# Optimization experiments

Measured on AMD Instinct MI355X. Metric: run time of the kernel, lower is better.

## Reference

```python
import jax, jax.numpy as jnp
import numpy as np

NUM_ATOMS = 100
D = 32        # initial_atom_dim
H = 16        # hidden_dim (multiplicity per irrep)
NB = 16       # edge_dim / number of bessel basis functions
CUT = 6.0     # radius_cutoff
DEG = 4.0     # degree_norm
OUT = 1       # output_dim
INV4PI = 1.0 / np.sqrt(4.0 * np.pi)  # 'integral' SH normalization


def _bessel(d, nb, cut):
    # e3nn soft_one_hot_linspace(basis='bessel', cutoff=True) * sqrt(nb)
    x = d[:, None]
    n = jnp.arange(1, nb + 1, dtype=d.dtype)
    safe = jnp.maximum(x, 1e-9)
    out = np.sqrt(2.0 / cut) * jnp.sin(n * jnp.pi * x / cut) / safe
    return out * (x < cut) * np.sqrt(float(nb))


def _fc(x, w1, w2):
    # e3nn FullyConnectedNet: fan-in normalized linear layers, silu, no bias
    h = jax.nn.silu(x @ w1 / np.sqrt(x.shape[-1]))
    return h @ w2 / np.sqrt(w1.shape[-1])


def _forward(atomic_numbers, edge_index, coords, atom_emb,
             fc0_w1, fc0_w2, fc1_w1, fc1_w2, w_readout):
    src, dst = edge_index[0], edge_index[1]
    N = coords.shape[0]
    E = src.shape[0]

    vec = coords[src] - coords[dst]                      # [E,3]
    dist = jnp.linalg.norm(vec, axis=-1)                 # [E]
    unit = vec / jnp.maximum(dist, 1e-9)[:, None]

    # spherical harmonics, l=0 and l=1, 'integral' normalization
    y0 = jnp.full((E,), INV4PI, dtype=coords.dtype)      # [E]
    y1 = (np.sqrt(3.0) * INV4PI) * unit                  # [E,3]
    basis = _bessel(dist, NB, CUT)                       # [E,NB]

    x = atom_emb[atomic_numbers]                         # [N,D] (row 0 is padding)

    # ---- layer 0: scalars (D x0e) x (1x0e+1x1o) -> H x0e + H x1o ----
    w = _fc(basis, fc0_w1, fc0_w2)                       # [E, 2*D*H] per-edge TP weights
    wa = w[:, : D * H].reshape(E, D, H)
    wb = w[:, D * H:].reshape(E, D, H)
    xs = x[src]
    n0 = 1.0 / np.sqrt(D)                                # path fan-in norm
    m0 = jnp.einsum('ed,edh->eh', xs, wa) * y0[:, None] * n0          # [E,H]
    m1 = jnp.einsum('ed,edh->eh', xs, wb)[:, :, None] * y1[:, None, :] * n0  # [E,H,3]
    z0 = jax.ops.segment_sum(m0, dst, num_segments=N) / DEG           # [N,H]
    z1 = jax.ops.segment_sum(m1, dst, num_segments=N) / DEG           # [N,H,3]

    # ---- layer 1: (H x0e + H x1o) x (1x0e+1x1o) -> same irreps, skip-connected ----
    w = _fc(basis, fc1_w1, fc1_w2)                       # [E, 4*H*H]
    w1_ = w[:, 0 * H * H:1 * H * H].reshape(E, H, H)     # 0e x 0e -> 0e
    w2_ = w[:, 1 * H * H:2 * H * H].reshape(E, H, H)     # 0e x 1o -> 1o
    w3_ = w[:, 2 * H * H:3 * H * H].reshape(E, H, H)     # 1o x 0e -> 1o
    w4_ = w[:, 3 * H * H:4 * H * H].reshape(E, H, H)     # 1o x 1o -> 0e (CG = dot/sqrt(3))
    s, v = z0[src], z1[src]
    n1 = 1.0 / np.sqrt(2 * H)                            # two paths per output irrep
    dot = jnp.einsum('ehm,em->eh', v, y1) / np.sqrt(3.0)
    o0 = (jnp.einsum('eh,ehk->ek', s, w1_) * y0[:, None]
          + jnp.einsum('eh,ehk->ek', dot, w4_)) * n1
    o1 = (jnp.einsum('eh,ehk->ek', s, w2_)[:, :, None] * y1[:, None, :]
          + jnp.einsum('ehm,ehk->ekm', v, w3_) * y0[:, None, None]) * n1
    z0 = jax.ops.segment_sum(o0, dst, num_segments=N) / DEG + z0      # skip
    z1 = jax.ops.segment_sum(o1, dst, num_segments=N) / DEG + z1

    # ---- scalar readout (o3.Linear onto 0e) + graph sum-pool ----
    node_scalar = z0 @ w_readout / np.sqrt(H)            # [N,OUT]
    return jnp.sum(node_scalar, axis=0)                  # [OUT]


def setup_inputs() -> dict:
    key = jax.random.key(0)
    ks = jax.random.split(key, 9)
    N, E = 10000, 160000
    atomic_numbers = jax.random.randint(ks[0], (N,), 0, NUM_ATOMS)
    coords = jax.random.normal(ks[1], (N, 3), dtype=jnp.float32)
    edge_index = jax.random.randint(ks[2], (2, E), 0, N)
    atom_emb = jax.random.normal(ks[3], (NUM_ATOMS, D), dtype=jnp.float32).at[0].set(0.0)
    fc0_w1 = jax.random.normal(ks[4], (NB, H), dtype=jnp.float32)
    fc0_w2 = jax.random.normal(ks[5], (H, 2 * D * H), dtype=jnp.float32)
    fc1_w1 = jax.random.normal(ks[6], (NB, H), dtype=jnp.float32)
    fc1_w2 = jax.random.normal(ks[7], (H, 4 * H * H), dtype=jnp.float32)
    w_readout = jax.random.normal(ks[8], (H, OUT), dtype=jnp.float32)
    return {"atomic_numbers": atomic_numbers, "coords": coords, "edge_index": edge_index,
            "atom_emb": atom_emb, "fc0_w1": fc0_w1, "fc0_w2": fc0_w2,
            "fc1_w1": fc1_w1, "fc1_w2": fc1_w2, "w_readout": w_readout}


def reference(atomic_numbers, coords, edge_index, atom_emb,
              fc0_w1, fc0_w2, fc1_w1, fc1_w2, w_readout):
    return _forward(atomic_numbers, edge_index, coords, atom_emb,
                    fc0_w1, fc0_w2, fc1_w1, fc1_w2, w_readout)
```

## Files before the change

### kernel.cpp

```cpp
#include <hip/hip_runtime.h>
#include <math.h>


namespace {
constexpr int   NATOMS   = 100;
constexpr int   CAP      = 64;
constexpr float PI_F     = 3.14159265358979323846f;
constexpr float INV4PI_F = 0.28209479177387814f;
constexpr float SQRT3_F  = 1.7320508075688772f;
constexpr float CUT_F    = 6.0f;
constexpr float BASIS_C  = 2.3094010767585034f;
constexpr float N0_F     = 0.17677669529663687f;
constexpr float K0_F = INV4PI_F * N0_F * 0.0625f;
constexpr float K1_F = SQRT3_F * INV4PI_F * N0_F * 0.0625f;
}

__device__ __forceinline__ float silu_fast(float x) {
  return x / (1.0f + __expf(-x));
}

__device__ __forceinline__ float block_reduce_sum(float v) {
  #pragma unroll
  for (int o = 32; o > 0; o >>= 1) v += __shfl_down(v, o, 64);
  __shared__ float ls[8];
  int lane = threadIdx.x & 63;
  int w    = threadIdx.x >> 6;
  if (lane == 0) ls[w] = v;
  __syncthreads();
  float s = 0.f;
  if (threadIdx.x == 0) {
    int nw = (blockDim.x + 63) >> 6;
    for (int i = 0; i < nw; ++i) s += ls[i];
  }
  return s;
}

__global__ void setup_kernel(const float* __restrict__ atom_emb,
                             const float* __restrict__ fc0_w2,
                             const float* __restrict__ fc1_w2,
                             const float* __restrict__ w_readout,
                             const int* __restrict__ ei,
                             const float* __restrict__ coords,
                             const int* __restrict__ an,
                             float* __restrict__ T0, float* __restrict__ T1,
                             float* __restrict__ G1T, float* __restrict__ G4T,
                             int* __restrict__ cursor,
                             float4* __restrict__ evec,
                             float4* __restrict__ ebuf,
                             int* __restrict__ ea,
                             int E) {
  int b = blockIdx.x;
  int tt = threadIdx.x;
  if (b < NATOMS) {
    int j = tt >> 4;
    int h = tt & 15;
    float s0 = 0.f, s1 = 0.f;
    #pragma unroll
    for (int d = 0; d < 32; ++d) {
      float x = atom_emb[b * 32 + d];
      s0 = fmaf(x, fc0_w2[j * 1024 + d * 16 + h], s0);
      s1 = fmaf(x, fc0_w2[j * 1024 + 512 + d * 16 + h], s1);
    }
    T0[b * 256 + tt] = s0;
    T1[b * 256 + tt] = s1;
  } else if (b == NATOMS) {
    int j = tt >> 4;
    int h = tt & 15;
    float g1 = 0.f, g4 = 0.f;
    #pragma unroll
    for (int k = 0; k < 16; ++k) {
      float r = w_readout[k];
      g1 = fmaf(fc1_w2[j * 1024 + h * 16 + k], r, g1);
      g4 = fmaf(fc1_w2[j * 1024 + 768 + h * 16 + k], r, g4);
    }
    G1T[h * 16 + j] = g1;
    G4T[h * 16 + j] = g4;
  } else {
    int e = (b - NATOMS - 1) * blockDim.x + tt;
    if (e < E) {
      int s = ei[e];
      int d = ei[E + e];
      float vx = coords[3 * s + 0] - coords[3 * d + 0];
      float vy = coords[3 * s + 1] - coords[3 * d + 1];
      float vz = coords[3 * s + 2] - coords[3 * d + 2];
      float dist = sqrtf(vx * vx + vy * vy + vz * vz);
      float inv  = 1.0f / fmaxf(dist, 1e-9f);
      float4 rec = make_float4(vx * inv, vy * inv, vz * inv, dist);
      evec[e] = rec;
      int pos = atomicAdd(&cursor[d], 1);
      if (pos < CAP) {
        ebuf[d * CAP + pos] = rec;
        ea[d * CAP + pos]   = an[s];
      }
    }
  }
}

__global__ void __launch_bounds__(256, 4)
gather_kernel(const float4* __restrict__ ebuf,
              const int* __restrict__ ea,
              const int* __restrict__ cursor,
              const float* __restrict__ fc0_w1,
              const float* __restrict__ T0,
              const float* __restrict__ T1,
              const float* __restrict__ G1T,
              const float* __restrict__ G4T,
              const float* __restrict__ w_readout,
              float* __restrict__ zbuf,
              float* __restrict__ out,
              int N) {
  __shared__ float ggs[512];
  ggs[threadIdx.x]       = G1T[threadIdx.x];
  ggs[256 + threadIdx.x] = G4T[threadIdx.x];
  __syncthreads();

  int wave = threadIdx.x >> 6;
  int lane = threadIdx.x & 63;
  int g    = lane >> 4;
  int t    = lane & 15;
  int base = lane & 48;
  int node = blockIdx.x * 4 + wave;
  bool valid = node < N;

  float w0c[16];
  #pragma unroll
  for (int k = 0; k < 16; ++k) w0c[k] = fc0_w1[k * 16 + t];
  float rr = w_readout[t];

  int cnt = valid ? min(cursor[node], CAP) : 0;
  int nb  = (valid ? node : 0) * CAP;

  const float angc = PI_F / CUT_F;
  float acc0 = 0.f, accx = 0.f, accy = 0.f, accz = 0.f;

  for (int i = g; i < cnt; i += 4) {
    float4 ev = ebuf[nb + i];
    int    a  = ea[nb + i];
    float dist = ev.w;
    float bc = (dist < CUT_F) ? (BASIS_C / fmaxf(dist, 1e-9f)) : 0.0f;

    float ang = angc * dist;
    float sc = __sinf(ang);
    float tw = 2.0f * __cosf(ang);
    float sp = 0.f, acc = 0.f;
    #pragma unroll
    for (int k = 0; k < 16; ++k) {
      acc = fmaf(sc, w0c[k], acc);
      float sn = fmaf(tw, sc, -sp);
      sp = sc; sc = sn;
    }
    float h0t = silu_fast(acc * bc * 0.25f);

    const float* t0 = T0 + a * 256 + t;
    const float* t1 = T1 + a * 256 + t;
    float u0 = 0.f, u1 = 0.f;
    #pragma unroll
    for (int j = 0; j < 16; ++j) {
      float hj = __shfl(h0t, base + j, 64);
      u0 = fmaf(hj, t0[j * 16], u0);
      u1 = fmaf(hj, t1[j * 16], u1);
    }
    acc0 += u0;
    accx = fmaf(u1, ev.x, accx);
    accy = fmaf(u1, ev.y, accy);
    accz = fmaf(u1, ev.z, accz);
  }

  acc0 += __shfl_xor(acc0, 16, 64); acc0 += __shfl_xor(acc0, 32, 64);
  accx += __shfl_xor(accx, 16, 64); accx += __shfl_xor(accx, 32, 64);
  accy += __shfl_xor(accy, 16, 64); accy += __shfl_xor(accy, 32, 64);
  accz += __shfl_xor(accz, 16, 64); accz += __shfl_xor(accz, 32, 64);

  float srcv = (g == 0) ? acc0 * K0_F
                        : ((g == 1) ? accx : (g == 2) ? accy : accz) * K1_F;
  int tofs = (g == 0) ? 0 : 256;
  float o = 0.f;
  #pragma unroll
  for (int h = 0; h < 16; ++h) {
    float vh = __shfl(srcv, base + h, 64);
    o = fmaf(ggs[tofs + h * 16 + t], vh, o);
  }
  if (valid) zbuf[(size_t)node * 64 + t * 4 + g] = o;

  float p = (valid && g == 0) ? acc0 * K0_F * rr : 0.f;
  float tot = block_reduce_sum(p);
  if (threadIdx.x == 0) atomicAdd(out, tot * 0.25f);
}

__global__ void __launch_bounds__(256, 4)
phase2_kernel(const int* __restrict__ ei,
              const float4* __restrict__ evec,
              const float* __restrict__ fc1_w1,
              const float* __restrict__ zbuf,
              float* __restrict__ out,
              int E) {
  int t = threadIdx.x & 15;
  float w1c[16];
  #pragma unroll
  for (int k = 0; k < 16; ++k) w1c[k] = fc1_w1[k * 16 + t];

  int gid = (blockIdx.x * blockDim.x + threadIdx.x) >> 4;
  int ngroups = (gridDim.x * blockDim.x) >> 4;
  const float angc = PI_F / CUT_F;

  float c = 0.f;
  for (int e = gid; e < E; e += ngroups) {
    int s = ei[e];
    float4 ev = evec[e];
    float dist = ev.w;
    float bc = (dist < CUT_F) ? (BASIS_C / fmaxf(dist, 1e-9f)) : 0.0f;

    float ang = angc * dist;
    float sc = __sinf(ang);
    float tw = 2.0f * __cosf(ang);
    float sp = 0.f, acc = 0.f;
    #pragma unroll
    for (int k = 0; k < 16; ++k) {
      acc = fmaf(sc, w1c[k], acc);
      float sn = fmaf(tw, sc, -sp);
      sp = sc; sc = sn;
    }
    float h1t = silu_fast(acc * bc * 0.25f);

    float4 z = ((const float4*)(zbuf + (size_t)s * 64))[t];
    c = fmaf(h1t, fmaf(z.y, ev.x, fmaf(z.z, ev.y, fmaf(z.w, ev.z, z.x))), c);
  }
  c *= INV4PI_F * N0_F * (1.0f / 64.0f);
  float tot = block_reduce_sum(c);
  if (threadIdx.x == 0) atomicAdd(out, tot);
}

extern "C" void kernel_launch(void* const* d_in, const int* in_sizes, int n_in,
                              void* d_out, int out_size, void* d_ws, size_t ws_size,
                              hipStream_t stream) {
  const int*   an        = (const int*)d_in[0];
  const float* coords    = (const float*)d_in[1];
  const int*   ei        = (const int*)d_in[2];
  const float* atom_emb  = (const float*)d_in[3];
  const float* fc0_w1    = (const float*)d_in[4];
  const float* fc0_w2    = (const float*)d_in[5];
  const float* fc1_w1    = (const float*)d_in[6];
  const float* fc1_w2    = (const float*)d_in[7];
  const float* w_readout = (const float*)d_in[8];

  int N = in_sizes[0];
  int E = in_sizes[2] / 2;

  float*  ws   = (float*)d_ws;
  float*  zbuf = ws;
  float4* evec = (float4*)(zbuf + (size_t)N * 64);
  float4* ebuf = evec + E;
  float*  T0   = (float*)(ebuf + (size_t)N * CAP);
  float*  T1   = T0 + NATOMS * 256;
  float*  G1T  = T1 + NATOMS * 256;
  float*  G4T  = G1T + 256;
  int*    cursor = (int*)(G4T + 256);
  int*    ea     = cursor + N;
  float*  out = (float*)d_out;

  hipMemsetAsync(cursor, 0, (size_t)N * sizeof(int), stream);
  hipMemsetAsync(out, 0, sizeof(float), stream);

  int blk = 256;
  int ebkts = (E + blk - 1) / blk;
  setup_kernel<<<NATOMS + 1 + ebkts, blk, 0, stream>>>(
      atom_emb, fc0_w2, fc1_w2, w_readout, ei, coords, an,
      T0, T1, G1T, G4T, cursor, evec, ebuf, ea, E);

  gather_kernel<<<(N + 3) / 4, blk, 0, stream>>>(
      ebuf, ea, cursor, fc0_w1, T0, T1, G1T, G4T, w_readout, zbuf, out, N);

  phase2_kernel<<<2048, blk, 0, stream>>>(ei, evec, fc1_w1, zbuf, out, E);
}
```

Baseline: 161.5 us.

## Split layer-0 message computation into edge-parallel kernel with per-node index gather

Per-edge layer-0 messages (Bessel basis, radial MLP, atom-type contraction, SH scaling) are computed in a new edge-parallel kernel and written to a per-edge message buffer. The node kernel then gathers these messages by edge index instead of recomputing them per node. The two per-type tables are interleaved into one float2-readable table. This aims to remove per-node load imbalance and underused lanes, at the cost of an extra launch and a large intermediate buffer round trip through memory.

```diff
diff --git a/kernel.cpp b/kernel.cpp
--- a/kernel.cpp
+++ b/kernel.cpp
@@ -42,12 +42,12 @@
                              const int* __restrict__ ei,
                              const float* __restrict__ coords,
                              const int* __restrict__ an,
-                             float* __restrict__ T0, float* __restrict__ T1,
+                             float* __restrict__ TI,
                              float* __restrict__ G1T, float* __restrict__ G4T,
                              int* __restrict__ cursor,
                              float4* __restrict__ evec,
-                             float4* __restrict__ ebuf,
                              int* __restrict__ ea,
+                             int* __restrict__ elist,
                              int E) {
   int b = blockIdx.x;
   int tt = threadIdx.x;
@@ -61,8 +61,8 @@
       s0 = fmaf(x, fc0_w2[j * 1024 + d * 16 + h], s0);
       s1 = fmaf(x, fc0_w2[j * 1024 + 512 + d * 16 + h], s1);
     }
-    T0[b * 256 + tt] = s0;
-    T1[b * 256 + tt] = s1;
+    TI[b * 512 + j * 32 + 2 * h]     = s0;
+    TI[b * 512 + j * 32 + 2 * h + 1] = s1;
   } else if (b == NATOMS) {
     int j = tt >> 4;
     int h = tt & 15;
@@ -85,30 +85,81 @@
       float vz = coords[3 * s + 2] - coords[3 * d + 2];
       float dist = sqrtf(vx * vx + vy * vy + vz * vz);
       float inv  = 1.0f / fmaxf(dist, 1e-9f);
-      float4 rec = make_float4(vx * inv, vy * inv, vz * inv, dist);
-      evec[e] = rec;
+      evec[e] = make_float4(vx * inv, vy * inv, vz * inv, dist);
+      ea[e] = an[s];
       int pos = atomicAdd(&cursor[d], 1);
-      if (pos < CAP) {
-        ebuf[d * CAP + pos] = rec;
-        ea[d * CAP + pos]   = an[s];
+      if (pos < CAP) elist[d * CAP + pos] = e;
+    }
+  }
+}
+
+__global__ void __launch_bounds__(256)
+m_kernel(const float4* __restrict__ evec,
+         const int* __restrict__ ea,
+         const float* __restrict__ TI,
+         const float* __restrict__ fc0_w1,
+         float4* __restrict__ mbuf,
+         int E) {
+  __shared__ float w1s[256];
+  w1s[threadIdx.x] = fc0_w1[threadIdx.x];
+  __syncthreads();
+  int lane = threadIdx.x & 63;
+  int g    = threadIdx.x >> 4;
+  int t    = threadIdx.x & 15;
+  int base = lane & 48;
+
+  float w0c[16];
+  #pragma unroll
+  for (int k = 0; k < 16; ++k) w0c[k] = w1s[k * 16 + t];
+
+  const float angc = PI_F / CUT_F;
+  int e = blockIdx.x * 32 + g;
+  #pragma unroll
+  for (int rep = 0; rep < 2; ++rep, e += 16) {
+    if (e < E) {
+      float4 ev = evec[e];
+      int    a  = ea[e];
+      float dist = ev.w;
+      float bc = (dist < CUT_F) ? (BASIS_C / fmaxf(dist, 1e-9f)) : 0.0f;
+
+      float ang = angc * dist;
+      float sc = __sinf(ang);
+      float tw = 2.0f * __cosf(ang);
+      float sp = 0.f, acc = 0.f;
+      #pragma unroll
+      for (int k = 0; k < 16; ++k) {
+        acc = fmaf(sc, w0c[k], acc);
+        float sn = fmaf(tw, sc, -sp);
+        sp = sc; sc = sn;
       }
+      float h0t = silu_fast(acc * bc * 0.25f);
+
+      const float2* tp = (const float2*)(TI + a * 512) + t;
+      float u0 = 0.f, u1 = 0.f;
+      #pragma unroll
+      for (int j = 0; j < 16; ++j) {
+        float hj = __shfl(h0t, base + j, 64);
+        float2 T = tp[j * 16];
+        u0 = fmaf(hj, T.x, u0);
+        u1 = fmaf(hj, T.y, u1);
+      }
+      float m1 = K1_F * u1;
+      mbuf[(size_t)e * 16 + t] =
+          make_float4(K0_F * u0, m1 * ev.x, m1 * ev.y, m1 * ev.z);
     }
   }
 }
 
 __global__ void __launch_bounds__(256, 4)
-gather_kernel(const float4* __restrict__ ebuf,
-              const int* __restrict__ ea,
-              const int* __restrict__ cursor,
-              const float* __restrict__ fc0_w1,
-              const float* __restrict__ T0,
-              const float* __restrict__ T1,
-              const float* __restrict__ G1T,
-              const float* __restrict__ G4T,
-              const float* __restrict__ w_readout,
-              float* __restrict__ zbuf,
-              float* __restrict__ out,
-              int N) {
+node_kernel(const int* __restrict__ elist,
+            const int* __restrict__ cursor,
+            const float4* __restrict__ mbuf,
+            const float* __restrict__ G1T,
+            const float* __restrict__ G4T,
+            const float* __restrict__ w_readout,
+            float* __restrict__ zbuf,
+            float* __restrict__ out,
+            int N) {
   __shared__ float ggs[512];
   ggs[threadIdx.x]       = G1T[threadIdx.x];
   ggs[256 + threadIdx.x] = G4T[threadIdx.x];
@@ -122,57 +173,23 @@
   int node = blockIdx.x * 4 + wave;
   bool valid = node < N;
 
-  float w0c[16];
-  #pragma unroll
-  for (int k = 0; k < 16; ++k) w0c[k] = fc0_w1[k * 16 + t];
   float rr = w_readout[t];
-
   int cnt = valid ? min(cursor[node], CAP) : 0;
-  int nb  = (valid ? node : 0) * CAP;
-
-  const float angc = PI_F / CUT_F;
-  float acc0 = 0.f, accx = 0.f, accy = 0.f, accz = 0.f;
-
+  const int* eb = elist + (size_t)(valid ? node : 0) * CAP;
+
+  float a0 = 0.f, ax = 0.f, ay = 0.f, az = 0.f;
   for (int i = g; i < cnt; i += 4) {
-    float4 ev = ebuf[nb + i];
-    int    a  = ea[nb + i];
-    float dist = ev.w;
-    float bc = (dist < CUT_F) ? (BASIS_C / fmaxf(dist, 1e-9f)) : 0.0f;
-
-    float ang = angc * dist;
-    float sc = __sinf(ang);
-    float tw = 2.0f * __cosf(ang);
-    float sp = 0.f, acc = 0.f;
-    #pragma unroll
-    for (int k = 0; k < 16; ++k) {
-      acc = fmaf(sc, w0c[k], acc);
-      float sn = fmaf(tw, sc, -sp);
-      sp = sc; sc = sn;
-    }
-    float h0t = silu_fast(acc * bc * 0.25f);
-
-    const float* t0 = T0 + a * 256 + t;
-    const float* t1 = T1 + a * 256 + t;
-    float u0 = 0.f, u1 = 0.f;
-    #pragma unroll
-    for (int j = 0; j < 16; ++j) {
-      float hj = __shfl(h0t, base + j, 64);
-      u0 = fmaf(hj, t0[j * 16], u0);
-      u1 = fmaf(hj, t1[j * 16], u1);
-    }
-    acc0 += u0;
-    accx = fmaf(u1, ev.x, accx);
-    accy = fmaf(u1, ev.y, accy);
-    accz = fmaf(u1, ev.z, accz);
-  }
-
-  acc0 += __shfl_xor(acc0, 16, 64); acc0 += __shfl_xor(acc0, 32, 64);
-  accx += __shfl_xor(accx, 16, 64); accx += __shfl_xor(accx, 32, 64);
-  accy += __shfl_xor(accy, 16, 64); accy += __shfl_xor(accy, 32, 64);
-  accz += __shfl_xor(accz, 16, 64); accz += __shfl_xor(accz, 32, 64);
-
-  float srcv = (g == 0) ? acc0 * K0_F
-                        : ((g == 1) ? accx : (g == 2) ? accy : accz) * K1_F;
+    int eidx = eb[i];
+    float4 f = mbuf[(size_t)eidx * 16 + t];
+    a0 += f.x; ax += f.y; ay += f.z; az += f.w;
+  }
+
+  a0 += __shfl_xor(a0, 16, 64); a0 += __shfl_xor(a0, 32, 64);
+  ax += __shfl_xor(ax, 16, 64); ax += __shfl_xor(ax, 32, 64);
+  ay += __shfl_xor(ay, 16, 64); ay += __shfl_xor(ay, 32, 64);
+  az += __shfl_xor(az, 16, 64); az += __shfl_xor(az, 32, 64);
+
+  float srcv = (g == 0) ? a0 : ((g == 1) ? ax : (g == 2) ? ay : az);
   int tofs = (g == 0) ? 0 : 256;
   float o = 0.f;
   #pragma unroll
@@ -182,7 +199,7 @@
   }
   if (valid) zbuf[(size_t)node * 64 + t * 4 + g] = o;
 
-  float p = (valid && g == 0) ? acc0 * K0_F * rr : 0.f;
+  float p = (valid && g == 0) ? a0 * rr : 0.f;
   float tot = block_reduce_sum(p);
   if (threadIdx.x == 0) atomicAdd(out, tot * 0.25f);
 }
@@ -246,16 +263,15 @@
   int N = in_sizes[0];
   int E = in_sizes[2] / 2;
 
-  float*  ws   = (float*)d_ws;
-  float*  zbuf = ws;
-  float4* evec = (float4*)(zbuf + (size_t)N * 64);
-  float4* ebuf = evec + E;
-  float*  T0   = (float*)(ebuf + (size_t)N * CAP);
-  float*  T1   = T0 + NATOMS * 256;
-  float*  G1T  = T1 + NATOMS * 256;
+  float4* evec = (float4*)d_ws;
+  float4* mbuf = evec + E;
+  float*  zbuf = (float*)(mbuf + (size_t)E * 16);
+  float*  TI   = zbuf + (size_t)N * 64;
+  float*  G1T  = TI + NATOMS * 512;
   float*  G4T  = G1T + 256;
   int*    cursor = (int*)(G4T + 256);
   int*    ea     = cursor + N;
+  int*    elist  = ea + E;
   float*  out = (float*)d_out;
 
   hipMemsetAsync(cursor, 0, (size_t)N * sizeof(int), stream);
@@ -265,10 +281,12 @@
   int ebkts = (E + blk - 1) / blk;
   setup_kernel<<<NATOMS + 1 + ebkts, blk, 0, stream>>>(
       atom_emb, fc0_w2, fc1_w2, w_readout, ei, coords, an,
-      T0, T1, G1T, G4T, cursor, evec, ebuf, ea, E);
-
-  gather_kernel<<<(N + 3) / 4, blk, 0, stream>>>(
-      ebuf, ea, cursor, fc0_w1, T0, T1, G1T, G4T, w_readout, zbuf, out, N);
+      TI, G1T, G4T, cursor, evec, ea, elist, E);
+
+  m_kernel<<<(E + 31) / 32, blk, 0, stream>>>(evec, ea, TI, fc0_w1, mbuf, E);
+
+  node_kernel<<<(N + 3) / 4, blk, 0, stream>>>(
+      elist, cursor, mbuf, G1T, G4T, w_readout, zbuf, out, N);
 
   phase2_kernel<<<2048, blk, 0, stream>>>(ei, evec, fc1_w1, zbuf, out, E);
 }
```

Result: slower. 187.1 us (+15.8%).
